# Kernel optimization log

Measured on AMD Instinct MI355X. Metric: run time of the kernel, lower is better.

Reference implementation:

```python
import jax, jax.numpy as jnp
import numpy as np

RANK = 8
LORA_ALPHA = 16
SCALING = LORA_ALPHA / RANK  # 2.0
POOL, IN_DIM, OUT_DIM = 16, 2048, 2048
B, S = 16, 2048


def setup_inputs() -> dict:
    key = jax.random.key(0)
    k_x, k_idx, k_a, k_b = jax.random.split(key, 4)
    x = jax.random.normal(k_x, (B, S, IN_DIM), dtype=jnp.float32)
    idx = jax.random.randint(k_idx, (B,), 0, POOL, dtype=jnp.int64)
    # Learned params: torch inits lora_b to zeros, but we use random values so the
    # output / gradients are non-trivial for correctness testing.
    lora_a = jax.random.normal(k_a, (POOL, IN_DIM, RANK), dtype=jnp.float32)
    lora_b = jax.random.normal(k_b, (POOL, RANK, OUT_DIM), dtype=jnp.float32)
    return {"x": x, "idx": idx, "lora_a": lora_a, "lora_b": lora_b}


def reference(x, idx, lora_a, lora_b):
    # Gather per-example adapters from the pool.
    a = lora_a[idx]  # [B, IN_DIM, RANK]
    b = lora_b[idx]  # [B, RANK, OUT_DIM]
    # Mathematically identical to x @ (a @ b), but avoids the [B, IN, OUT]
    # intermediate: contract through the low rank first.
    xa = jnp.einsum('bsi,bir->bsr', x, a)       # [B, S, RANK]
    out = jnp.einsum('bsr,bro->bso', xa, b)     # [B, S, OUT_DIM]
    return out * SCALING
```

## Files before the change

### kernel.cpp

```cpp
#include <hip/hip_runtime.h>


constexpr int IN_DIM  = 2048;
constexpr int OUT_DIM = 2048;
constexpr int RANK    = 8;
constexpr int S_LEN   = 2048;
constexpr int B_SZ    = 16;
constexpr int ROWS    = 4;
constexpr int SC      = 16;
constexpr int NPH     = SC / ROWS;
constexpr float SCALING = 2.0f;

__global__ __launch_bounds__(256, 2) void lora_fused_v2(
    const float* __restrict__ x,
    const int*   __restrict__ idx,
    const float* __restrict__ la,
    const float* __restrict__ lb,
    float*       __restrict__ out)
{
    const int t    = threadIdx.x;
    const int lane = t & 63;
    const int wave = t >> 6;

    constexpr int BLOCKS_PER_B = S_LEN / SC;
    const int b   = blockIdx.x / BLOCKS_PER_B;
    const int s0  = (blockIdx.x % BLOCKS_PER_B) * SC;
    const int pid = idx[b];

    float a_reg[8][RANK];
    {
        const float* ap0 = la + ((size_t)pid * IN_DIM + (size_t)t * 4) * RANK;
        const float* ap1 = ap0 + (size_t)1024 * RANK;
        #pragma unroll
        for (int j = 0; j < 4; ++j) {
            float4 v0 = *reinterpret_cast<const float4*>(ap0 + j * RANK);
            float4 v1 = *reinterpret_cast<const float4*>(ap0 + j * RANK + 4);
            a_reg[j][0]=v0.x; a_reg[j][1]=v0.y; a_reg[j][2]=v0.z; a_reg[j][3]=v0.w;
            a_reg[j][4]=v1.x; a_reg[j][5]=v1.y; a_reg[j][6]=v1.z; a_reg[j][7]=v1.w;
            float4 w0 = *reinterpret_cast<const float4*>(ap1 + j * RANK);
            float4 w1 = *reinterpret_cast<const float4*>(ap1 + j * RANK + 4);
            a_reg[4+j][0]=w0.x; a_reg[4+j][1]=w0.y; a_reg[4+j][2]=w0.z; a_reg[4+j][3]=w0.w;
            a_reg[4+j][4]=w1.x; a_reg[4+j][5]=w1.y; a_reg[4+j][6]=w1.z; a_reg[4+j][7]=w1.w;
        }
    }
    float b_reg[RANK][8];
    {
        const float* bp = lb + (size_t)pid * RANK * OUT_DIM + (size_t)t * 4;
        #pragma unroll
        for (int r = 0; r < RANK; ++r) {
            float4 v0 = *reinterpret_cast<const float4*>(bp + (size_t)r * OUT_DIM);
            float4 v1 = *reinterpret_cast<const float4*>(bp + (size_t)r * OUT_DIM + 1024);
            b_reg[r][0]=v0.x; b_reg[r][1]=v0.y; b_reg[r][2]=v0.z; b_reg[r][3]=v0.w;
            b_reg[r][4]=v1.x; b_reg[r][5]=v1.y; b_reg[r][6]=v1.z; b_reg[r][7]=v1.w;
        }
    }

    __shared__ float red[2][4][ROWS][RANK];

    const float* xbase = x   + ((size_t)b * S_LEN + s0) * IN_DIM;
    float*       obase = out + ((size_t)b * S_LEN + s0) * OUT_DIM;

    float4 xbuf[2][ROWS][2];
    #pragma unroll
    for (int row = 0; row < ROWS; ++row) {
        xbuf[0][row][0] = *reinterpret_cast<const float4*>(xbase + (size_t)row * IN_DIM + t * 4);
        xbuf[0][row][1] = *reinterpret_cast<const float4*>(xbase + (size_t)row * IN_DIM + 1024 + t * 4);
    }

    #pragma unroll
    for (int p = 0; p < NPH; ++p) {
        const int cur = p & 1;

        if (p + 1 < NPH) {
            #pragma unroll
            for (int row = 0; row < ROWS; ++row) {
                const size_t s = (size_t)(p + 1) * ROWS + row;
                xbuf[cur ^ 1][row][0] = *reinterpret_cast<const float4*>(xbase + s * IN_DIM + t * 4);
                xbuf[cur ^ 1][row][1] = *reinterpret_cast<const float4*>(xbase + s * IN_DIM + 1024 + t * 4);
            }
        }

        float acc[ROWS][RANK];
        #pragma unroll
        for (int row = 0; row < ROWS; ++row) {
            #pragma unroll
            for (int r = 0; r < RANK; ++r) acc[row][r] = 0.0f;
            float4 xlo = xbuf[cur][row][0];
            float4 xhi = xbuf[cur][row][1];
            float xv[8] = {xlo.x, xlo.y, xlo.z, xlo.w, xhi.x, xhi.y, xhi.z, xhi.w};
            #pragma unroll
            for (int j = 0; j < 8; ++j)
                #pragma unroll
                for (int r = 0; r < RANK; ++r)
                    acc[row][r] = fmaf(xv[j], a_reg[j][r], acc[row][r]);
        }

        float m4[ROWS][4];
        {
            const bool hi = lane & 1;
            #pragma unroll
            for (int row = 0; row < ROWS; ++row)
                #pragma unroll
                for (int j = 0; j < 4; ++j) {
                    float send = hi ? acc[row][j] : acc[row][j + 4];
                    float keep = hi ? acc[row][j + 4] : acc[row][j];
                    m4[row][j] = keep + __shfl_xor(send, 1);
                }
        }
        float m2[ROWS][2];
        {
            const bool hi = lane & 2;
            #pragma unroll
            for (int row = 0; row < ROWS; ++row)
                #pragma unroll
                for (int j = 0; j < 2; ++j) {
                    float send = hi ? m2[0][0] : 0.0f;
                    (void)send;
                    float snd = hi ? m4[row][j] : m4[row][j + 2];
                    float kp  = hi ? m4[row][j + 2] : m4[row][j];
                    m2[row][j] = kp + __shfl_xor(snd, 2);
                }
        }
        float m1[ROWS];
        {
            const bool hi = lane & 4;
            #pragma unroll
            for (int row = 0; row < ROWS; ++row) {
                float snd = hi ? m2[row][0] : m2[row][1];
                float kp  = hi ? m2[row][1] : m2[row][0];
                m1[row] = kp + __shfl_xor(snd, 4);
            }
        }
        float w2[2];
        {
            const bool hi = lane & 8;
            #pragma unroll
            for (int j = 0; j < 2; ++j) {
                float snd = hi ? m1[j] : m1[j + 2];
                float kp  = hi ? m1[j + 2] : m1[j];
                w2[j] = kp + __shfl_xor(snd, 8);
            }
        }
        float w1;
        {
            const bool hi = lane & 16;
            float snd = hi ? w2[0] : w2[1];
            float kp  = hi ? w2[1] : w2[0];
            w1 = kp + __shfl_xor(snd, 16);
        }
        w1 += __shfl_xor(w1, 32);

        const int rOf   = ((lane & 1) << 2) | (lane & 2) | ((lane >> 2) & 1);
        const int rowOf = ((lane >> 2) & 2) | ((lane >> 4) & 1);
        if (lane < 32) red[cur][wave][rowOf][rOf] = w1;
        __syncthreads();

        #pragma unroll
        for (int row = 0; row < ROWS; ++row) {
            float4 lo = *reinterpret_cast<const float4*>(&red[cur][0][row][0]);
            float4 hi = *reinterpret_cast<const float4*>(&red[cur][0][row][4]);
            #pragma unroll
            for (int w = 1; w < 4; ++w) {
                float4 l2 = *reinterpret_cast<const float4*>(&red[cur][w][row][0]);
                float4 h2 = *reinterpret_cast<const float4*>(&red[cur][w][row][4]);
                lo.x += l2.x; lo.y += l2.y; lo.z += l2.z; lo.w += l2.w;
                hi.x += h2.x; hi.y += h2.y; hi.z += h2.z; hi.w += h2.w;
            }
            float xsv[RANK] = {SCALING * lo.x, SCALING * lo.y, SCALING * lo.z, SCALING * lo.w,
                               SCALING * hi.x, SCALING * hi.y, SCALING * hi.z, SCALING * hi.w};

            float ov[8];
            #pragma unroll
            for (int j = 0; j < 8; ++j) ov[j] = 0.0f;
            #pragma unroll
            for (int r = 0; r < RANK; ++r)
                #pragma unroll
                for (int j = 0; j < 8; ++j)
                    ov[j] = fmaf(xsv[r], b_reg[r][j], ov[j]);

            float* orow = obase + ((size_t)p * ROWS + row) * OUT_DIM;
            *reinterpret_cast<float4*>(orow + t * 4)        = make_float4(ov[0], ov[1], ov[2], ov[3]);
            *reinterpret_cast<float4*>(orow + 1024 + t * 4) = make_float4(ov[4], ov[5], ov[6], ov[7]);
        }
    }
}

extern "C" void kernel_launch(void* const* d_in, const int* in_sizes, int n_in,
                              void* d_out, int out_size, void* d_ws, size_t ws_size,
                              hipStream_t stream) {
    const float* x   = (const float*)d_in[0];
    const int*   idx = (const int*)  d_in[1];
    const float* la  = (const float*)d_in[2];
    const float* lb  = (const float*)d_in[3];
    float* out = (float*)d_out;

    dim3 grid(B_SZ * (S_LEN / SC));
    lora_fused_v2<<<grid, 256, 0, stream>>>(x, idx, la, lb, out);
}
```

Baseline: 115.0 us.

## Software-pipeline rank reduction and output stage, use nontemporal stores, double rows per block

Restructures the phase loop so the output projection and store for phase q-1 run after the x-projection for phase q. The shared-memory reduction barrier moves ahead of the write, leaving one barrier per phase, and that barrier now also protects buffer reuse. Output stores become nontemporal to avoid polluting cache, and rows per block double from 16 to 32, halving the grid and the per-block reloads of adapter registers. The cost is fewer blocks, which may hurt latency hiding and occupancy balance across CUs.

Result: faster. 97.24 us (-15.4%).

```diff
diff --git a/kernel.cpp b/kernel.cpp
--- a/kernel.cpp
+++ b/kernel.cpp
@@ -1,5 +1,7 @@
 #include <hip/hip_runtime.h>
 
+
+typedef float f32x4 __attribute__((ext_vector_type(4)));
 
 constexpr int IN_DIM  = 2048;
 constexpr int OUT_DIM = 2048;
@@ -7,11 +9,11 @@
 constexpr int S_LEN   = 2048;
 constexpr int B_SZ    = 16;
 constexpr int ROWS    = 4;
-constexpr int SC      = 16;
+constexpr int SC      = 32;
 constexpr int NPH     = SC / ROWS;
 constexpr float SCALING = 2.0f;
 
-__global__ __launch_bounds__(256, 2) void lora_fused_v2(
+__global__ __launch_bounds__(256, 2) void lora_fused_v3(
     const float* __restrict__ x,
     const int*   __restrict__ idx,
     const float* __restrict__ la,
@@ -67,16 +69,44 @@
         xbuf[0][row][1] = *reinterpret_cast<const float4*>(xbase + (size_t)row * IN_DIM + 1024 + t * 4);
     }
 
-    #pragma unroll
-    for (int p = 0; p < NPH; ++p) {
-        const int cur = p & 1;
-
-        if (p + 1 < NPH) {
+    auto stage2_store = [&](int p, int rb) {
+        #pragma unroll
+        for (int row = 0; row < ROWS; ++row) {
+            float4 lo = *reinterpret_cast<const float4*>(&red[rb][0][row][0]);
+            float4 hi = *reinterpret_cast<const float4*>(&red[rb][0][row][4]);
+            #pragma unroll
+            for (int w = 1; w < 4; ++w) {
+                float4 l2 = *reinterpret_cast<const float4*>(&red[rb][w][row][0]);
+                float4 h2 = *reinterpret_cast<const float4*>(&red[rb][w][row][4]);
+                lo.x += l2.x; lo.y += l2.y; lo.z += l2.z; lo.w += l2.w;
+                hi.x += h2.x; hi.y += h2.y; hi.z += h2.z; hi.w += h2.w;
+            }
+            float xsv[RANK] = {SCALING*lo.x, SCALING*lo.y, SCALING*lo.z, SCALING*lo.w,
+                               SCALING*hi.x, SCALING*hi.y, SCALING*hi.z, SCALING*hi.w};
+            float ov[8];
+            #pragma unroll
+            for (int j = 0; j < 8; ++j) ov[j] = 0.0f;
+            #pragma unroll
+            for (int r = 0; r < RANK; ++r)
+                #pragma unroll
+                for (int j = 0; j < 8; ++j)
+                    ov[j] = fmaf(xsv[r], b_reg[r][j], ov[j]);
+
+            float* orow = obase + ((size_t)p * ROWS + row) * OUT_DIM;
+            f32x4 o0 = {ov[0], ov[1], ov[2], ov[3]};
+            f32x4 o1 = {ov[4], ov[5], ov[6], ov[7]};
+            __builtin_nontemporal_store(o0, reinterpret_cast<f32x4*>(orow + t * 4));
+            __builtin_nontemporal_store(o1, reinterpret_cast<f32x4*>(orow + 1024 + t * 4));
+        }
+    };
+
+    auto phase = [&](int q, int cb) {
+        if (q + 1 < NPH) {
             #pragma unroll
             for (int row = 0; row < ROWS; ++row) {
-                const size_t s = (size_t)(p + 1) * ROWS + row;
-                xbuf[cur ^ 1][row][0] = *reinterpret_cast<const float4*>(xbase + s * IN_DIM + t * 4);
-                xbuf[cur ^ 1][row][1] = *reinterpret_cast<const float4*>(xbase + s * IN_DIM + 1024 + t * 4);
+                const size_t s = (size_t)(q + 1) * ROWS + row;
+                xbuf[cb ^ 1][row][0] = *reinterpret_cast<const float4*>(xbase + s * IN_DIM + t * 4);
+                xbuf[cb ^ 1][row][1] = *reinterpret_cast<const float4*>(xbase + s * IN_DIM + 1024 + t * 4);
             }
         }
 
@@ -85,8 +115,8 @@
         for (int row = 0; row < ROWS; ++row) {
             #pragma unroll
             for (int r = 0; r < RANK; ++r) acc[row][r] = 0.0f;
-            float4 xlo = xbuf[cur][row][0];
-            float4 xhi = xbuf[cur][row][1];
+            float4 xlo = xbuf[cb][row][0];
+            float4 xhi = xbuf[cb][row][1];
             float xv[8] = {xlo.x, xlo.y, xlo.z, xlo.w, xhi.x, xhi.y, xhi.z, xhi.w};
             #pragma unroll
             for (int j = 0; j < 8; ++j)
@@ -102,9 +132,9 @@
             for (int row = 0; row < ROWS; ++row)
                 #pragma unroll
                 for (int j = 0; j < 4; ++j) {
-                    float send = hi ? acc[row][j] : acc[row][j + 4];
-                    float keep = hi ? acc[row][j + 4] : acc[row][j];
-                    m4[row][j] = keep + __shfl_xor(send, 1);
+                    float snd = hi ? acc[row][j] : acc[row][j + 4];
+                    float kp  = hi ? acc[row][j + 4] : acc[row][j];
+                    m4[row][j] = kp + __shfl_xor(snd, 1);
                 }
         }
         float m2[ROWS][2];
@@ -114,8 +144,6 @@
             for (int row = 0; row < ROWS; ++row)
                 #pragma unroll
                 for (int j = 0; j < 2; ++j) {
-                    float send = hi ? m2[0][0] : 0.0f;
-                    (void)send;
                     float snd = hi ? m4[row][j] : m4[row][j + 2];
                     float kp  = hi ? m4[row][j + 2] : m4[row][j];
                     m2[row][j] = kp + __shfl_xor(snd, 2);
@@ -150,39 +178,23 @@
         }
         w1 += __shfl_xor(w1, 32);
 
+        __syncthreads();
+
         const int rOf   = ((lane & 1) << 2) | (lane & 2) | ((lane >> 2) & 1);
         const int rowOf = ((lane >> 2) & 2) | ((lane >> 4) & 1);
-        if (lane < 32) red[cur][wave][rowOf][rOf] = w1;
-        __syncthreads();
-
-        #pragma unroll
-        for (int row = 0; row < ROWS; ++row) {
-            float4 lo = *reinterpret_cast<const float4*>(&red[cur][0][row][0]);
-            float4 hi = *reinterpret_cast<const float4*>(&red[cur][0][row][4]);
-            #pragma unroll
-            for (int w = 1; w < 4; ++w) {
-                float4 l2 = *reinterpret_cast<const float4*>(&red[cur][w][row][0]);
-                float4 h2 = *reinterpret_cast<const float4*>(&red[cur][w][row][4]);
-                lo.x += l2.x; lo.y += l2.y; lo.z += l2.z; lo.w += l2.w;
-                hi.x += h2.x; hi.y += h2.y; hi.z += h2.z; hi.w += h2.w;
-            }
-            float xsv[RANK] = {SCALING * lo.x, SCALING * lo.y, SCALING * lo.z, SCALING * lo.w,
-                               SCALING * hi.x, SCALING * hi.y, SCALING * hi.z, SCALING * hi.w};
-
-            float ov[8];
-            #pragma unroll
-            for (int j = 0; j < 8; ++j) ov[j] = 0.0f;
-            #pragma unroll
-            for (int r = 0; r < RANK; ++r)
-                #pragma unroll
-                for (int j = 0; j < 8; ++j)
-                    ov[j] = fmaf(xsv[r], b_reg[r][j], ov[j]);
-
-            float* orow = obase + ((size_t)p * ROWS + row) * OUT_DIM;
-            *reinterpret_cast<float4*>(orow + t * 4)        = make_float4(ov[0], ov[1], ov[2], ov[3]);
-            *reinterpret_cast<float4*>(orow + 1024 + t * 4) = make_float4(ov[4], ov[5], ov[6], ov[7]);
-        }
-    }
+        if (lane < 32) red[cb][wave][rowOf][rOf] = w1;
+
+        if (q >= 1) stage2_store(q - 1, cb ^ 1);
+    };
+
+    #pragma unroll
+    for (int q = 0; q < NPH; q += 2) {
+        phase(q, 0);
+        phase(q + 1, 1);
+    }
+
+    __syncthreads();
+    stage2_store(NPH - 1, (NPH - 1) & 1);
 }
 
 extern "C" void kernel_launch(void* const* d_in, const int* in_sizes, int n_in,
@@ -195,5 +207,5 @@
     float* out = (float*)d_out;
 
     dim3 grid(B_SZ * (S_LEN / SC));
-    lora_fused_v2<<<grid, 256, 0, stream>>>(x, idx, la, lb, out);
+    lora_fused_v3<<<grid, 256, 0, stream>>>(x, idx, la, lb, out);
 }
```
